# Performance work log

Measured on AMD Instinct MI355X. Metric: run time of the kernel, lower is better.

The kernel has to match this reference:

```python
import jax, jax.numpy as jnp
import numpy as np

DIM = 2048
DIM_HEAD = 64
HEADS = 16
FF_MULT = 4
LORA_R = 8
ATTN_INNER = DIM_HEAD * HEADS            # 1024
FF_INNER = DIM * FF_MULT                 # 8192
FUSED_DIMS = (ATTN_INNER, DIM_HEAD, DIM_HEAD, FF_INNER * 2)
B, N = 2, 2048


def setup_inputs() -> dict:
    key = jax.random.key(0)
    ks = jax.random.split(key, 12)
    s = 0.02
    inp = {
        "x": jax.random.normal(ks[0], (B, N, DIM), dtype=jnp.float32),
        "gamma": jnp.ones((DIM,), dtype=jnp.float32),
        "w_fused": jax.random.normal(ks[1], (DIM, sum(FUSED_DIMS)), dtype=jnp.float32) * s,
        "w_attn_out": jax.random.normal(ks[2], (ATTN_INNER, DIM), dtype=jnp.float32) * s,
        "w_ff_out": jax.random.normal(ks[3], (FF_INNER, DIM), dtype=jnp.float32) * s,
        "lora_q_a": jax.random.normal(ks[4], (DIM, LORA_R), dtype=jnp.float32) * s,
        "lora_q_b": jax.random.normal(ks[5], (LORA_R, ATTN_INNER), dtype=jnp.float32) * s,
        "lora_k_a": jax.random.normal(ks[6], (DIM, LORA_R), dtype=jnp.float32) * s,
        "lora_k_b": jax.random.normal(ks[7], (LORA_R, DIM_HEAD), dtype=jnp.float32) * s,
        "lora_v_a": jax.random.normal(ks[8], (DIM, LORA_R), dtype=jnp.float32) * s,
        "lora_v_b": jax.random.normal(ks[9], (LORA_R, DIM_HEAD), dtype=jnp.float32) * s,
        "lora_o_a": jax.random.normal(ks[10], (ATTN_INNER, LORA_R), dtype=jnp.float32) * s,
        "lora_o_b": jax.random.normal(ks[11], (LORA_R, DIM), dtype=jnp.float32) * s,
    }
    return inp


def _rotate_half(x):
    x1, x2 = jnp.split(x, 2, axis=-1)
    return jnp.concatenate((-x2, x1), axis=-1)


def _rope(pos, t):
    return t * jnp.cos(pos) + _rotate_half(t) * jnp.sin(pos)


def _forward(x, gamma, w_fused, w_attn_out, w_ff_out,
             lora_q_a, lora_q_b, lora_k_a, lora_k_b,
             lora_v_a, lora_v_b, lora_o_a, lora_o_b):
    b, n, d = x.shape
    # LayerNorm (beta = 0)
    mu = jnp.mean(x, axis=-1, keepdims=True)
    var = jnp.var(x, axis=-1, keepdims=True)
    xn = (x - mu) * jax.lax.rsqrt(var + 1e-5) * gamma

    fused = xn @ w_fused
    i0, i1, i2 = np.cumsum(FUSED_DIMS)[:3]
    q, k, v, ff = fused[..., :i0], fused[..., i0:i1], fused[..., i1:i2], fused[..., i2:]

    # LoRA additive terms
    q = q + (xn @ lora_q_a) @ lora_q_b
    k = k + (xn @ lora_k_a) @ lora_k_b
    v = v + (xn @ lora_v_a) @ lora_v_b

    q = q.reshape(b, n, HEADS, DIM_HEAD).transpose(0, 2, 1, 3)  # b h n d
    q = q * (DIM_HEAD ** -0.5)

    # rotary embedding: pos (n, dim_head)
    inv_freq = 1.0 / (10000.0 ** (jnp.arange(0, DIM_HEAD, 2, dtype=jnp.float32) / DIM_HEAD))
    freqs = jnp.arange(n, dtype=jnp.float32)[:, None] * inv_freq[None, :]
    pos = jnp.concatenate((freqs, freqs), axis=-1)
    q = _rope(pos, q)
    k = _rope(pos, k)  # k is b n d (multi-query, single kv head)

    sim = jnp.einsum('bhid,bjd->bhij', q, k)
    causal = jnp.triu(jnp.ones((n, n), dtype=bool), k=1)
    sim = jnp.where(causal, -jnp.finfo(sim.dtype).max, sim)
    attn = jax.nn.softmax(sim, axis=-1)
    out = jnp.einsum('bhij,bjd->bhid', attn, v)
    out = out.transpose(0, 2, 1, 3).reshape(b, n, ATTN_INNER)

    attn_out = out @ w_attn_out + (out @ lora_o_a) @ lora_o_b

    # SwiGLU: chunk -> (x_ff, gate); silu(gate) * x_ff
    x_ff, gate = jnp.split(ff, 2, axis=-1)
    ff_out = (jax.nn.silu(gate) * x_ff) @ w_ff_out

    return attn_out + ff_out


def reference(x, gamma, w_fused, w_attn_out, w_ff_out,
              lora_q_a, lora_q_b, lora_k_a, lora_k_b,
              lora_v_a, lora_v_b, lora_o_a, lora_o_b):
    return _forward(x, gamma, w_fused, w_attn_out, w_ff_out,
                    lora_q_a, lora_q_b, lora_k_a, lora_k_b,
                    lora_v_a, lora_v_b, lora_o_a, lora_o_b)
```

## Files before the change

### kernel.cpp

```cpp
#include <hip/hip_runtime.h>
#include <cstdint>


typedef __bf16 bf16_t;
typedef __bf16 bf16x8 __attribute__((ext_vector_type(8)));
typedef float f32x4 __attribute__((ext_vector_type(4)));

#define LOG2E 1.44269504088896340736f
#define LOG2_10K 13.287712379549449f

__device__ __forceinline__ void gload_lds16(const void* g, void* l) {
  __builtin_amdgcn_global_load_lds(
      (__attribute__((address_space(1))) void*)(uintptr_t)g,
      (__attribute__((address_space(3))) void*)(uint32_t)(uintptr_t)l,
      16, 0, 0);
}

__device__ __forceinline__ f32x4 mfma16(bf16x8 a, bf16x8 b, f32x4 c) {
  return __builtin_amdgcn_mfma_f32_16x16x32_bf16(a, b, c, 0, 0, 0);
}

__global__ __launch_bounds__(256) void ln_kernel(
    const float* __restrict__ x, const float* __restrict__ gamma,
    bf16_t* __restrict__ xn)
{
  const int row = blockIdx.x;
  const int t = threadIdx.x;
  const float4* xr = (const float4*)(x + (size_t)row * 2048);
  float4 a = xr[t * 2];
  float4 b = xr[t * 2 + 1];
  float s  = a.x + a.y + a.z + a.w + b.x + b.y + b.z + b.w;
  float ss = a.x*a.x + a.y*a.y + a.z*a.z + a.w*a.w
           + b.x*b.x + b.y*b.y + b.z*b.z + b.w*b.w;
  #pragma unroll
  for (int m = 1; m < 64; m <<= 1) {
    s  += __shfl_xor(s, m);
    ss += __shfl_xor(ss, m);
  }
  __shared__ float red[8];
  const int wave = t >> 6, lane = t & 63;
  if (lane == 0) { red[wave] = s; red[4 + wave] = ss; }
  __syncthreads();
  const float stot  = red[0] + red[1] + red[2] + red[3];
  const float sstot = red[4] + red[5] + red[6] + red[7];
  const float mu  = stot * (1.f / 2048.f);
  const float var = sstot * (1.f / 2048.f) - mu * mu;
  const float rs  = rsqrtf(var + 1e-5f);
  float v[8] = {a.x, a.y, a.z, a.w, b.x, b.y, b.z, b.w};
  bf16x8 o;
  #pragma unroll
  for (int e = 0; e < 8; ++e)
    o[e] = (bf16_t)((v[e] - mu) * rs * gamma[t * 8 + e]);
  *(bf16x8*)(xn + (size_t)row * 2048 + t * 8) = o;
}

__global__ __launch_bounds__(256) void transpose_wf_kernel(
    const float* __restrict__ w,
    const float* __restrict__ qa, const float* __restrict__ qb,
    const float* __restrict__ ka, const float* __restrict__ kb,
    const float* __restrict__ va, const float* __restrict__ vb,
    bf16_t* __restrict__ wfT)
{
  __shared__ float tile[64][65];
  const int t  = threadIdx.x;
  const int n0 = blockIdx.x * 64;
  const int k0 = blockIdx.y * 64;
  #pragma unroll
  for (int it = 0; it < 4; ++it) {
    const int kr = (t >> 4) + it * 16;
    const float4 vv = *(const float4*)(w + (size_t)(k0 + kr) * 17536 + n0 + (t & 15) * 4);
    tile[kr][(t & 15) * 4 + 0] = vv.x;
    tile[kr][(t & 15) * 4 + 1] = vv.y;
    tile[kr][(t & 15) * 4 + 2] = vv.z;
    tile[kr][(t & 15) * 4 + 3] = vv.w;
  }
  __syncthreads();
  const float* la = nullptr; const float* lb = nullptr;
  int nbo = 0, ldlb = 0;
  if (n0 < 1024)      { la = qa; lb = qb; nbo = n0;        ldlb = 1024; }
  else if (n0 < 1088) { la = ka; lb = kb; nbo = n0 - 1024; ldlb = 64;   }
  else if (n0 < 1152) { la = va; lb = vb; nbo = n0 - 1088; ldlb = 64;   }
  #pragma unroll
  for (int it = 0; it < 2; ++it) {
    const int nl = (t >> 3) + it * 32;
    const int kl = (t & 7) * 8;
    float vals[8];
    #pragma unroll
    for (int e = 0; e < 8; ++e) vals[e] = tile[kl + e][nl];
    if (la) {
      float bc[8];
      #pragma unroll
      for (int r = 0; r < 8; ++r) bc[r] = lb[r * ldlb + nbo + nl];
      #pragma unroll
      for (int e = 0; e < 8; ++e) {
        const float* ar = la + (size_t)(k0 + kl + e) * 8;
        float d = 0.f;
        #pragma unroll
        for (int r = 0; r < 8; ++r) d += ar[r] * bc[r];
        vals[e] += d;
      }
    }
    bf16x8 o;
    #pragma unroll
    for (int e = 0; e < 8; ++e) o[e] = (bf16_t)vals[e];
    *(bf16x8*)(wfT + (size_t)(n0 + nl) * 2048 + k0 + kl) = o;
  }
}

__global__ __launch_bounds__(256) void transpose_w2_kernel(
    const float* __restrict__ wff,
    const float* __restrict__ watt,
    const float* __restrict__ oa, const float* __restrict__ ob,
    bf16_t* __restrict__ w2T)
{
  __shared__ float tile[64][65];
  const int t  = threadIdx.x;
  const int n0 = blockIdx.x * 64;
  const int k0 = blockIdx.y * 64;
  const bool isatt = (k0 >= 8192);
  const float* src = isatt ? (watt + (size_t)(k0 - 8192) * 2048)
                           : (wff + (size_t)k0 * 2048);
  #pragma unroll
  for (int it = 0; it < 4; ++it) {
    const int kr = (t >> 4) + it * 16;
    const float4 vv = *(const float4*)(src + (size_t)kr * 2048 + n0 + (t & 15) * 4);
    tile[kr][(t & 15) * 4 + 0] = vv.x;
    tile[kr][(t & 15) * 4 + 1] = vv.y;
    tile[kr][(t & 15) * 4 + 2] = vv.z;
    tile[kr][(t & 15) * 4 + 3] = vv.w;
  }
  __syncthreads();
  #pragma unroll
  for (int it = 0; it < 2; ++it) {
    const int nl = (t >> 3) + it * 32;
    const int kl = (t & 7) * 8;
    float vals[8];
    #pragma unroll
    for (int e = 0; e < 8; ++e) vals[e] = tile[kl + e][nl];
    if (isatt) {
      float bc[8];
      #pragma unroll
      for (int r = 0; r < 8; ++r) bc[r] = ob[r * 2048 + n0 + nl];
      #pragma unroll
      for (int e = 0; e < 8; ++e) {
        const float* ar = oa + (size_t)(k0 - 8192 + kl + e) * 8;
        float d = 0.f;
        #pragma unroll
        for (int r = 0; r < 8; ++r) d += ar[r] * bc[r];
        vals[e] += d;
      }
    }
    bf16x8 o;
    #pragma unroll
    for (int e = 0; e < 8; ++e) o[e] = (bf16_t)vals[e];
    *(bf16x8*)(w2T + (size_t)(n0 + nl) * 9216 + k0 + kl) = o;
  }
}

__device__ __forceinline__ void gemm_core_128x128(
    const bf16_t* __restrict__ A, int ldA, int m0,
    const bf16_t* __restrict__ BT, int ldB, int n0,
    int K, bf16_t* As, bf16_t* Bs, f32x4* acc)
{
  const int t = threadIdx.x;
  const int wave = t >> 6;
  const int lane = t & 63;
  const int quad = lane >> 4;
  const int ln15 = lane & 15;
  const int wm = wave & 1, wn = wave >> 1;

  const bf16_t* gA = A + (size_t)(m0 + (t >> 2)) * ldA + ((t & 3) << 3);
  const bf16_t* gB = BT + (size_t)(n0 + (t >> 2)) * ldB + ((t & 3) << 3);
  char* lA = (char*)As + wave * 1024;
  char* lB = (char*)Bs + wave * 1024;
  const size_t sA64 = (size_t)64 * ldA;
  const size_t sB64 = (size_t)64 * ldB;
  const int aoff = (wm * 64 + ln15) * 32 + quad * 8;
  const int boff = (wn * 64 + ln15) * 32 + quad * 8;

  for (int kt = 0; kt < K; kt += 32) {
    gload_lds16(gA,        lA);
    gload_lds16(gA + sA64, lA + 4096);
    gload_lds16(gB,        lB);
    gload_lds16(gB + sB64, lB + 4096);
    gA += 32;
    gB += 32;
    __syncthreads();
    bf16x8 a0 = *(const bf16x8*)(As + aoff);
    bf16x8 a1 = *(const bf16x8*)(As + aoff + 512);
    bf16x8 a2 = *(const bf16x8*)(As + aoff + 1024);
    bf16x8 a3 = *(const bf16x8*)(As + aoff + 1536);
    bf16x8 b0 = *(const bf16x8*)(Bs + boff);
    bf16x8 b1 = *(const bf16x8*)(Bs + boff + 512);
    bf16x8 b2 = *(const bf16x8*)(Bs + boff + 1024);
    bf16x8 b3 = *(const bf16x8*)(Bs + boff + 1536);
    acc[0]  = mfma16(a0, b0, acc[0]);
    acc[1]  = mfma16(a0, b1, acc[1]);
    acc[2]  = mfma16(a0, b2, acc[2]);
    acc[3]  = mfma16(a0, b3, acc[3]);
    acc[4]  = mfma16(a1, b0, acc[4]);
    acc[5]  = mfma16(a1, b1, acc[5]);
    acc[6]  = mfma16(a1, b2, acc[6]);
    acc[7]  = mfma16(a1, b3, acc[7]);
    acc[8]  = mfma16(a2, b0, acc[8]);
    acc[9]  = mfma16(a2, b1, acc[9]);
    acc[10] = mfma16(a2, b2, acc[10]);
    acc[11] = mfma16(a2, b3, acc[11]);
    acc[12] = mfma16(a3, b0, acc[12]);
    acc[13] = mfma16(a3, b1, acc[13]);
    acc[14] = mfma16(a3, b2, acc[14]);
    acc[15] = mfma16(a3, b3, acc[15]);
    __syncthreads();
  }
}

__device__ __forceinline__ void gemm_core_dual(
    const bf16_t* gA, const bf16_t* gB0, const bf16_t* gB1,
    int ldA, int ldB, int K,
    bf16_t* As, bf16_t* B0s, bf16_t* B1s,
    f32x4* acc0, f32x4* acc1)
{
  const int t = threadIdx.x;
  const int wave = t >> 6;
  const int lane = t & 63;
  const int quad = lane >> 4;
  const int ln15 = lane & 15;
  const int wm = wave & 1, wn = wave >> 1;

  char* lA = (char*)As + wave * 1024;
  char* l0 = (char*)B0s + wave * 1024;
  char* l1 = (char*)B1s + wave * 1024;
  const size_t sA64 = (size_t)64 * ldA;
  const size_t sB64 = (size_t)64 * ldB;
  const int aoff = (wm * 64 + ln15) * 32 + quad * 8;
  const int boff = (wn * 64 + ln15) * 32 + quad * 8;

  for (int kt = 0; kt < K; kt += 32) {
    gload_lds16(gA,         lA);
    gload_lds16(gA + sA64,  lA + 4096);
    gload_lds16(gB0,        l0);
    gload_lds16(gB0 + sB64, l0 + 4096);
    gload_lds16(gB1,        l1);
    gload_lds16(gB1 + sB64, l1 + 4096);
    gA += 32; gB0 += 32; gB1 += 32;
    __syncthreads();
    bf16x8 a0 = *(const bf16x8*)(As + aoff);
    bf16x8 a1 = *(const bf16x8*)(As + aoff + 512);
    bf16x8 a2 = *(const bf16x8*)(As + aoff + 1024);
    bf16x8 a3 = *(const bf16x8*)(As + aoff + 1536);
    bf16x8 p0 = *(const bf16x8*)(B0s + boff);
    bf16x8 p1 = *(const bf16x8*)(B0s + boff + 512);
    bf16x8 p2 = *(const bf16x8*)(B0s + boff + 1024);
    bf16x8 p3 = *(const bf16x8*)(B0s + boff + 1536);
    bf16x8 q0 = *(const bf16x8*)(B1s + boff);
    bf16x8 q1 = *(const bf16x8*)(B1s + boff + 512);
    bf16x8 q2 = *(const bf16x8*)(B1s + boff + 1024);
    bf16x8 q3 = *(const bf16x8*)(B1s + boff + 1536);
    acc0[0]  = mfma16(a0, p0, acc0[0]);
    acc0[1]  = mfma16(a0, p1, acc0[1]);
    acc0[2]  = mfma16(a0, p2, acc0[2]);
    acc0[3]  = mfma16(a0, p3, acc0[3]);
    acc1[0]  = mfma16(a0, q0, acc1[0]);
    acc1[1]  = mfma16(a0, q1, acc1[1]);
    acc1[2]  = mfma16(a0, q2, acc1[2]);
    acc1[3]  = mfma16(a0, q3, acc1[3]);
    acc0[4]  = mfma16(a1, p0, acc0[4]);
    acc0[5]  = mfma16(a1, p1, acc0[5]);
    acc0[6]  = mfma16(a1, p2, acc0[6]);
    acc0[7]  = mfma16(a1, p3, acc0[7]);
    acc1[4]  = mfma16(a1, q0, acc1[4]);
    acc1[5]  = mfma16(a1, q1, acc1[5]);
    acc1[6]  = mfma16(a1, q2, acc1[6]);
    acc1[7]  = mfma16(a1, q3, acc1[7]);
    acc0[8]  = mfma16(a2, p0, acc0[8]);
    acc0[9]  = mfma16(a2, p1, acc0[9]);
    acc0[10] = mfma16(a2, p2, acc0[10]);
    acc0[11] = mfma16(a2, p3, acc0[11]);
    acc1[8]  = mfma16(a2, q0, acc1[8]);
    acc1[9]  = mfma16(a2, q1, acc1[9]);
    acc1[10] = mfma16(a2, q2, acc1[10]);
    acc1[11] = mfma16(a2, q3, acc1[11]);
    acc0[12] = mfma16(a3, p0, acc0[12]);
    acc0[13] = mfma16(a3, p1, acc0[13]);
    acc0[14] = mfma16(a3, p2, acc0[14]);
    acc0[15] = mfma16(a3, p3, acc0[15]);
    acc1[12] = mfma16(a3, q0, acc1[12]);
    acc1[13] = mfma16(a3, q1, acc1[13]);
    acc1[14] = mfma16(a3, q2, acc1[14]);
    acc1[15] = mfma16(a3, q3, acc1[15]);
    __syncthreads();
  }
}

__global__ __launch_bounds__(256, 2) void gemm1_qkv_kernel(
    const bf16_t* __restrict__ xn, const bf16_t* __restrict__ wfT,
    bf16_t* __restrict__ Q, bf16_t* __restrict__ K, bf16_t* __restrict__ Vt)
{
  __shared__ __align__(16) bf16_t As[128 * 32];
  __shared__ __align__(16) bf16_t B0s[128 * 32];
  __shared__ __align__(16) bf16_t B1s[128 * 32];
  const int m0 = blockIdx.x * 128;
  const int y = blockIdx.y;
  const int t = threadIdx.x;
  const int wave = t >> 6, lane = t & 63;
  const int quad = lane >> 4, ln15 = lane & 15;
  const int wm = wave & 1, wn = wave >> 1;

  const int rb = m0 + wm * 64 + quad * 4;
  const float invf0 = exp2f(-(float)ln15 * (LOG2_10K / 32.0f));
  const float invf1 = exp2f(-(float)(16 + ln15) * (LOG2_10K / 32.0f));

  if (y < 4) {
    const bf16_t* gA  = xn  + (size_t)(m0 + (t >> 2)) * 2048 + ((t & 3) << 3);
    const bf16_t* gB0 = wfT + (size_t)(y * 256 + (t >> 2)) * 2048 + ((t & 3) << 3);
    const bf16_t* gB1 = wfT + (size_t)(y * 256 + 128 + (t >> 2)) * 2048 + ((t & 3) << 3);
    f32x4 acc0[16], acc1[16];
    #pragma unroll
    for (int f = 0; f < 16; ++f) {
      acc0[f] = (f32x4){0.f, 0.f, 0.f, 0.f};
      acc1[f] = (f32x4){0.f, 0.f, 0.f, 0.f};
    }
    gemm_core_dual(gA, gB0, gB1, 2048, 2048, 2048, As, B0s, B1s, acc0, acc1);
    #pragma unroll
    for (int half = 0; half < 2; ++half) {
      const f32x4* acc = half ? acc1 : acc0;
      const int hd = y * 4 + half * 2 + wn;
      #pragma unroll
      for (int i = 0; i < 4; ++i) {
        #pragma unroll
        for (int rr = 0; rr < 4; ++rr) {
          const int row = rb + i * 16 + rr;
          const int b = row >> 11, n = row & 2047;
          const float fn = (float)n;
          float s0, c0, s1, c1;
          __sincosf(fn * invf0, &s0, &c0);
          __sincosf(fn * invf1, &s1, &c1);
          float vals[4];
          #pragma unroll
          for (int j = 0; j < 4; ++j) vals[j] = acc[i * 4 + j][rr];
          #pragma unroll
          for (int j = 0; j < 4; ++j) {
            const float rot = (j < 2) ? -vals[j + 2] : vals[j - 2];
            const float c = (j & 1) ? c1 : c0;
            const float s = (j & 1) ? s1 : s0;
            const float o = (vals[j] * c + rot * s) * 0.125f;
            Q[(((size_t)b * 16 + hd) * 2048 + n) * 64 + j * 16 + ln15] = (bf16_t)o;
          }
        }
      }
    }
  } else {
    f32x4 acc[16];
    #pragma unroll
    for (int f = 0; f < 16; ++f) acc[f] = (f32x4){0.f, 0.f, 0.f, 0.f};
    gemm_core_128x128(xn, 2048, m0, wfT, 2048, 1024, 2048, As, B0s, acc);
    const bool is_k = (wn == 0);
    #pragma unroll
    for (int i = 0; i < 4; ++i) {
      #pragma unroll
      for (int rr = 0; rr < 4; ++rr) {
        const int row = rb + i * 16 + rr;
        const int b = row >> 11, n = row & 2047;
        float vals[4];
        #pragma unroll
        for (int j = 0; j < 4; ++j) vals[j] = acc[i * 4 + j][rr];
        if (is_k) {
          const float fn = (float)n;
          float s0, c0, s1, c1;
          __sincosf(fn * invf0, &s0, &c0);
          __sincosf(fn * invf1, &s1, &c1);
          #pragma unroll
          for (int j = 0; j < 4; ++j) {
            const float rot = (j < 2) ? -vals[j + 2] : vals[j - 2];
            const float c = (j & 1) ? c1 : c0;
            const float s = (j & 1) ? s1 : s0;
            K[((size_t)b * 2048 + n) * 64 + j * 16 + ln15] = (bf16_t)(vals[j] * c + rot * s);
          }
        } else {
          #pragma unroll
          for (int j = 0; j < 4; ++j)
            Vt[((size_t)b * 64 + j * 16 + ln15) * 2048 + n] = (bf16_t)vals[j];
        }
      }
    }
  }
}

__global__ __launch_bounds__(256, 2) void gemm1_ff_kernel(
    const bf16_t* __restrict__ xn, const bf16_t* __restrict__ wfT,
    bf16_t* __restrict__ A2, int m_base)
{
  __shared__ __align__(16) bf16_t As[128 * 32];
  __shared__ __align__(16) bf16_t Bg[128 * 32];
  __shared__ __align__(16) bf16_t Bx[128 * 32];
  const int m0 = m_base + blockIdx.x * 128;
  const int c  = blockIdx.y;
  const int t = threadIdx.x;
  const int wave = t >> 6, lane = t & 63;
  const int quad = lane >> 4, ln15 = lane & 15;
  const int wm = wave & 1, wn = wave >> 1;

  const bf16_t* gA = xn  + (size_t)(m0 + (t >> 2)) * 2048 + ((t & 3) << 3);
  const bf16_t* gG = wfT + (size_t)(9344 + c * 128 + (t >> 2)) * 2048 + ((t & 3) << 3);
  const bf16_t* gX = wfT + (size_t)(1152 + c * 128 + (t >> 2)) * 2048 + ((t & 3) << 3);

  f32x4 accg[16], accx[16];
  #pragma unroll
  for (int f = 0; f < 16; ++f) {
    accg[f] = (f32x4){0.f, 0.f, 0.f, 0.f};
    accx[f] = (f32x4){0.f, 0.f, 0.f, 0.f};
  }
  gemm_core_dual(gA, gG, gX, 2048, 2048, 2048, As, Bg, Bx, accg, accx);

  const int rb = m0 + wm * 64 + quad * 4;
  const int cb = c * 128 + wn * 64 + ln15;
  #pragma unroll
  for (int i = 0; i < 4; ++i)
    #pragma unroll
    for (int rr = 0; rr < 4; ++rr) {
      bf16_t* dst = A2 + (size_t)(rb + i * 16 + rr) * 9216 + cb;
      #pragma unroll
      for (int j = 0; j < 4; ++j) {
        const float g = accg[i * 4 + j][rr];
        const float xv = accx[i * 4 + j][rr];
        dst[j * 16] = (bf16_t)(xv * (g / (1.f + exp2f(-g * LOG2E))));
      }
    }
}

__global__ __launch_bounds__(256, 2) void gemm2_kernel(
    const bf16_t* __restrict__ A2, const bf16_t* __restrict__ w2T,
    float* __restrict__ out)
{
  __shared__ __align__(16) bf16_t As[128 * 32];
  __shared__ __align__(16) bf16_t B0[128 * 32];
  __shared__ __align__(16) bf16_t B1[128 * 32];
  const int m0 = blockIdx.x * 128;
  const int n0 = blockIdx.y * 256;
  const int k0 = blockIdx.z * 4608;
  const int t = threadIdx.x;
  const int wave = t >> 6, lane = t & 63;
  const int quad = lane >> 4, ln15 = lane & 15;
  const int wm = wave & 1, wn = wave >> 1;

  const bf16_t* gA  = A2  + (size_t)(m0 + (t >> 2)) * 9216 + k0 + ((t & 3) << 3);
  const bf16_t* gB0 = w2T + (size_t)(n0 + (t >> 2)) * 9216 + k0 + ((t & 3) << 3);
  const bf16_t* gB1 = w2T + (size_t)(n0 + 128 + (t >> 2)) * 9216 + k0 + ((t & 3) << 3);

  f32x4 acc0[16], acc1[16];
  #pragma unroll
  for (int f = 0; f < 16; ++f) {
    acc0[f] = (f32x4){0.f, 0.f, 0.f, 0.f};
    acc1[f] = (f32x4){0.f, 0.f, 0.f, 0.f};
  }
  gemm_core_dual(gA, gB0, gB1, 9216, 9216, 4608, As, B0, B1, acc0, acc1);

  const int rb = m0 + wm * 64 + quad * 4;
  #pragma unroll
  for (int half = 0; half < 2; ++half) {
    const f32x4* acc = half ? acc1 : acc0;
    const int cb = n0 + half * 128 + wn * 64 + ln15;
    #pragma unroll
    for (int i = 0; i < 4; ++i)
      #pragma unroll
      for (int rr = 0; rr < 4; ++rr) {
        float* dst = out + (size_t)(rb + i * 16 + rr) * 2048 + cb;
        #pragma unroll
        for (int j = 0; j < 4; ++j)
          unsafeAtomicAdd(dst + j * 16, acc[i * 4 + j][rr]);
      }
  }
}

__global__ __launch_bounds__(256, 2) void attn_kernel(
    const bf16_t* __restrict__ Q, const bf16_t* __restrict__ Kg_,
    const bf16_t* __restrict__ Vt, bf16_t* __restrict__ A2)
{
  __shared__ __align__(16) bf16_t Qs[64 * 64];
  __shared__ __align__(16) bf16_t Ks[64 * 64];
  __shared__ __align__(16) bf16_t Vs[64 * 64];
  __shared__ __align__(16) bf16_t Ps[64 * 64];
  const int pidx = blockIdx.x, bh = blockIdx.y;
  const int b = bh >> 4, h = bh & 15;
  const int t = threadIdx.x;
  const int wave = t >> 6, lane = t & 63;
  const int quad = lane >> 4, ln15 = lane & 15;

  const bf16_t* Kg = Kg_ + (size_t)b * 2048 * 64;
  const bf16_t* Vg = Vt + (size_t)b * 64 * 2048;

  for (int hlf = 0; hlf < 2; ++hlf) {
    const int qt = hlf ? (31 - pidx) : pidx;
    const int qm0 = qt * 64;
    const bf16_t* Qg = Q + ((size_t)bh * 2048 + qm0) * 64;

    {
      const bf16_t* g = Qg + (size_t)(t >> 3) * 64 + ((t & 7) << 3);
      char* l = (char*)Qs + wave * 1024;
      gload_lds16(g,           l);
      gload_lds16(g + 32 * 64, l + 4096);
    }

    float mstate[4], lstate[4];
    f32x4 o_acc[4];
    #pragma unroll
    for (int rr = 0; rr < 4; ++rr) { mstate[rr] = -1e30f; lstate[rr] = 0.f; }
    #pragma unroll
    for (int jd = 0; jd < 4; ++jd) o_acc[jd] = (f32x4){0.f, 0.f, 0.f, 0.f};

    const int njt = qt + 1;
    for (int jt = 0; jt < njt; ++jt) {
      {
        const bf16_t* kg = Kg + (size_t)(jt * 64 + (t >> 3)) * 64 + ((t & 7) << 3);
        char* lk = (char*)Ks + wave * 1024;
        gload_lds16(kg,           lk);
        gload_lds16(kg + 32 * 64, lk + 4096);
        const bf16_t* vg = Vg + (size_t)(t >> 3) * 2048 + jt * 64 + ((t & 7) << 3);
        char* lv = (char*)Vs + wave * 1024;
        gload_lds16(vg,                   lv);
        gload_lds16(vg + (size_t)32*2048, lv + 4096);
      }
      __syncthreads();

      f32x4 sA[4];
      #pragma unroll
      for (int j = 0; j < 4; ++j) sA[j] = (f32x4){0.f, 0.f, 0.f, 0.f};
      #pragma unroll
      for (int ks = 0; ks < 2; ++ks) {
        bf16x8 aq = *(const bf16x8*)(Qs + (wave * 16 + ln15) * 64 + ks * 32 + quad * 8);
        #pragma unroll
        for (int j = 0; j < 4; ++j) {
          bf16x8 bk = *(const bf16x8*)(Ks + (j * 16 + ln15) * 64 + ks * 32 + quad * 8);
          sA[j] = mfma16(aq, bk, sA[j]);
        }
      }

      const bool needmask = (jt * 64 + 63 > qm0 + wave * 16);
      const int row0 = qm0 + wave * 16 + quad * 4;
      float alpha[4];
      #pragma unroll
      for (int rr = 0; rr < 4; ++rr) {
        const int rowg = row0 + rr;
        if (needmask) {
          #pragma unroll
          for (int j = 0; j < 4; ++j) {
            const int colg = jt * 64 + j * 16 + ln15;
            if (colg > rowg) sA[j][rr] = -1e30f;
          }
        }
        float mx = fmaxf(fmaxf(sA[0][rr], sA[1][rr]),
                         fmaxf(sA[2][rr], sA[3][rr]));
        mx = fmaxf(mx, __shfl_xor(mx, 1));
        mx = fmaxf(mx, __shfl_xor(mx, 2));
        mx = fmaxf(mx, __shfl_xor(mx, 4));
        mx = fmaxf(mx, __shfl_xor(mx, 8));
        const float mold = mstate[rr];
        const float mnew = fmaxf(mold, mx);
        const float al = exp2f((mold - mnew) * LOG2E);
        float rsum = 0.f;
        #pragma unroll
        for (int j = 0; j < 4; ++j) {
          const float p = exp2f((sA[j][rr] - mnew) * LOG2E);
          sA[j][rr] = p;
          rsum += p;
        }
        rsum += __shfl_xor(rsum, 1);
        rsum += __shfl_xor(rsum, 2);
        rsum += __shfl_xor(rsum, 4);
        rsum += __shfl_xor(rsum, 8);
        lstate[rr] = lstate[rr] * al + rsum;
        mstate[rr] = mnew;
        alpha[rr] = al;
      }
      #pragma unroll
      for (int jd = 0; jd < 4; ++jd)
        #pragma unroll
        for (int rr = 0; rr < 4; ++rr)
          o_acc[jd][rr] *= alpha[rr];
      #pragma unroll
      for (int j = 0; j < 4; ++j)
        #pragma unroll
        for (int rr = 0; rr < 4; ++rr)
          Ps[wave * 1024 + (quad * 4 + rr) * 64 + j * 16 + ln15] = (bf16_t)sA[j][rr];

      #pragma unroll
      for (int ks = 0; ks < 2; ++ks) {
        bf16x8 ap = *(const bf16x8*)(Ps + wave * 1024 + ln15 * 64 + ks * 32 + quad * 8);
        #pragma unroll
        for (int jd = 0; jd < 4; ++jd) {
          bf16x8 bv = *(const bf16x8*)(Vs + (jd * 16 + ln15) * 64 + ks * 32 + quad * 8);
          o_acc[jd] = mfma16(ap, bv, o_acc[jd]);
        }
      }
      __syncthreads();
    }

    const int row0 = qm0 + wave * 16 + quad * 4;
    #pragma unroll
    for (int rr = 0; rr < 4; ++rr) {
      const float inv = 1.f / lstate[rr];
      bf16_t* dst = A2 + ((size_t)b * 2048 + row0 + rr) * 9216 + 8192 + h * 64 + ln15;
      #pragma unroll
      for (int jd = 0; jd < 4; ++jd)
        dst[jd * 16] = (bf16_t)(o_acc[jd][rr] * inv);
    }
  }
}

extern "C" void kernel_launch(void* const* d_in, const int* in_sizes, int n_in,
                              void* d_out, int out_size, void* d_ws, size_t ws_size,
                              hipStream_t stream)
{
  const float* x      = (const float*)d_in[0];
  const float* gamma  = (const float*)d_in[1];
  const float* wfused = (const float*)d_in[2];
  const float* watt   = (const float*)d_in[3];
  const float* wff    = (const float*)d_in[4];
  const float* qa     = (const float*)d_in[5];
  const float* qb     = (const float*)d_in[6];
  const float* ka     = (const float*)d_in[7];
  const float* kb     = (const float*)d_in[8];
  const float* va     = (const float*)d_in[9];
  const float* vb     = (const float*)d_in[10];
  const float* oa     = (const float*)d_in[11];
  const float* ob     = (const float*)d_in[12];
  float* out = (float*)d_out;

  char* ws = (char*)d_ws;
  bf16_t* xn  = (bf16_t*)(ws);
  bf16_t* wfT = (bf16_t*)(ws + 16777216);
  bf16_t* w2T = (bf16_t*)(ws + 88604672);
  bf16_t* A2  = (bf16_t*)(ws + 126353408);
  bf16_t* Qr  = (bf16_t*)(ws + 201850880);
  bf16_t* Kr  = (bf16_t*)(ws + 210239488);
  bf16_t* Vtr = (bf16_t*)(ws + 210763776);

  hipMemsetAsync(d_out, 0, (size_t)out_size * sizeof(float), stream);

  ln_kernel<<<dim3(4096), dim3(256), 0, stream>>>(x, gamma, xn);
  transpose_wf_kernel<<<dim3(274, 32), dim3(256), 0, stream>>>(
      wfused, qa, qb, ka, kb, va, vb, wfT);
  transpose_w2_kernel<<<dim3(32, 144), dim3(256), 0, stream>>>(
      wff, watt, oa, ob, w2T);
  gemm1_qkv_kernel<<<dim3(32, 5), dim3(256), 0, stream>>>(xn, wfT, Qr, Kr, Vtr);
  gemm1_ff_kernel<<<dim3(16, 64), dim3(256), 0, stream>>>(xn, wfT, A2, 0);
  gemm1_ff_kernel<<<dim3(16, 64), dim3(256), 0, stream>>>(xn, wfT, A2, 2048);
  attn_kernel<<<dim3(16, 32), dim3(256), 0, stream>>>(Qr, Kr, Vtr, A2);
  gemm2_kernel<<<dim3(32, 8, 2), dim3(256), 0, stream>>>(A2, w2T, out);
}
```

Before: 964.4 us.

## Rewrite FF and output GEMMs with 256-row tiles, 4-stage LDS pipeline, no split-K

Both large GEMMs now use 512-thread blocks with 256-row M tiles and a 4-stage global-to-LDS pipeline driven by direct global_load_lds. The pipeline uses XOR-swizzled LDS layouts, raised wave priority around the MFMA blocks, and interleaved gate/x columns so each wave holds matching SwiGLU pairs. The two FF launches merge into one. The output GEMM drops split-K and its atomics in favour of plain stores, which also removes the memset of the output. The cost is large LDS use (128KB and 96KB per block), which limits occupancy, and fewer blocks in the output GEMM (256).

```diff
diff --git a/kernel.cpp b/kernel.cpp
--- a/kernel.cpp
+++ b/kernel.cpp
@@ -386,90 +386,192 @@
   }
 }
 
-__global__ __launch_bounds__(256, 2) void gemm1_ff_kernel(
+__global__ __launch_bounds__(512, 2) void gemm1_ff_kernel(
     const bf16_t* __restrict__ xn, const bf16_t* __restrict__ wfT,
-    bf16_t* __restrict__ A2, int m_base)
-{
-  __shared__ __align__(16) bf16_t As[128 * 32];
-  __shared__ __align__(16) bf16_t Bg[128 * 32];
-  __shared__ __align__(16) bf16_t Bx[128 * 32];
-  const int m0 = m_base + blockIdx.x * 128;
-  const int c  = blockIdx.y;
+    bf16_t* __restrict__ A2)
+{
+  __shared__ __align__(16) char lds[131072];
+  const int m0 = blockIdx.x * 256;
+  const int c0 = blockIdx.y * 128;
   const int t = threadIdx.x;
-  const int wave = t >> 6, lane = t & 63;
+  const int w = t >> 6, lane = t & 63;
   const int quad = lane >> 4, ln15 = lane & 15;
-  const int wm = wave & 1, wn = wave >> 1;
-
-  const bf16_t* gA = xn  + (size_t)(m0 + (t >> 2)) * 2048 + ((t & 3) << 3);
-  const bf16_t* gG = wfT + (size_t)(9344 + c * 128 + (t >> 2)) * 2048 + ((t & 3) << 3);
-  const bf16_t* gX = wfT + (size_t)(1152 + c * 128 + (t >> 2)) * 2048 + ((t & 3) << 3);
-
-  f32x4 accg[16], accx[16];
-  #pragma unroll
-  for (int f = 0; f < 16; ++f) {
-    accg[f] = (f32x4){0.f, 0.f, 0.f, 0.f};
-    accx[f] = (f32x4){0.f, 0.f, 0.f, 0.f};
-  }
-  gemm_core_dual(gA, gG, gX, 2048, 2048, 2048, As, Bg, Bx, accg, accx);
-
-  const int rb = m0 + wm * 64 + quad * 4;
-  const int cb = c * 128 + wn * 64 + ln15;
-  #pragma unroll
-  for (int i = 0; i < 4; ++i)
+  const int wm = w & 1, wn = w >> 1;
+
+  const int p  = w * 64 + lane;
+  const int r  = p >> 2;
+  const int cl = (p & 3) ^ ((r >> 1) & 3);
+  const bf16_t* gA = xn + (size_t)(m0 + r) * 2048 + cl * 8;
+  const int r2 = r + 128;
+  const int cm0 = c0 + ((r  >> 5) << 4) + (r  & 15);
+  const int cm1 = c0 + ((r2 >> 5) << 4) + (r2 & 15);
+  const int wr0 = ((r  >> 4) & 1) ? (1152 + cm0) : (9344 + cm0);
+  const int wr1 = ((r2 >> 4) & 1) ? (1152 + cm1) : (9344 + cm1);
+  const bf16_t* gB0 = wfT + (size_t)wr0 * 2048 + cl * 8;
+  const bf16_t* gB1 = wfT + (size_t)wr1 * 2048 + cl * 8;
+
+  const int ro = ln15 * 64 + ((quad ^ ((ln15 >> 1) & 3)) * 16);
+
+  f32x4 acc[8][4];
+  #pragma unroll
+  for (int mf = 0; mf < 8; ++mf)
+    #pragma unroll
+    for (int nf = 0; nf < 4; ++nf)
+      acc[mf][nf] = (f32x4){0.f, 0.f, 0.f, 0.f};
+
+  #pragma unroll
+  for (int pt = 0; pt < 3; ++pt) {
+    char* lA = lds + pt * 16384 + w * 1024;
+    gload_lds16(gA,                        lA);
+    gload_lds16(gA + (size_t)128 * 2048,   lA + 8192);
+    char* lB = lds + 65536 + pt * 16384 + w * 1024;
+    gload_lds16(gB0, lB);
+    gload_lds16(gB1, lB + 8192);
+    gA += 32; gB0 += 32; gB1 += 32;
+  }
+  asm volatile("s_waitcnt vmcnt(8)" ::: "memory");
+  __builtin_amdgcn_s_barrier();
+
+  for (int tt = 0; tt < 64; ++tt) {
+    const int s  = tt & 3;
+    const int s3 = (tt + 3) & 3;
+    const bool st = (tt < 61);
+    bf16x8 a[4], b[4];
+    #pragma unroll
+    for (int mf = 0; mf < 4; ++mf)
+      a[mf] = *(const bf16x8*)(lds + s * 16384 + wm * 8192 + mf * 1024 + ro);
+    #pragma unroll
+    for (int nf = 0; nf < 4; ++nf)
+      b[nf] = *(const bf16x8*)(lds + 65536 + s * 16384 + wn * 4096 + nf * 1024 + ro);
+    if (st) {
+      char* lA = lds + s3 * 16384 + w * 1024;
+      gload_lds16(gA,                      lA);
+      gload_lds16(gA + (size_t)128 * 2048, lA + 8192);
+    }
+    __builtin_amdgcn_s_barrier();
+    __builtin_amdgcn_s_setprio(1);
+    #pragma unroll
+    for (int mf = 0; mf < 4; ++mf)
+      #pragma unroll
+      for (int nf = 0; nf < 4; ++nf)
+        acc[mf][nf] = mfma16(a[mf], b[nf], acc[mf][nf]);
+    __builtin_amdgcn_s_setprio(0);
+    bf16x8 a2[4];
+    #pragma unroll
+    for (int mf = 0; mf < 4; ++mf)
+      a2[mf] = *(const bf16x8*)(lds + s * 16384 + wm * 8192 + (4 + mf) * 1024 + ro);
+    if (st) {
+      char* lB = lds + 65536 + s3 * 16384 + w * 1024;
+      gload_lds16(gB0, lB);
+      gload_lds16(gB1, lB + 8192);
+      gA += 32; gB0 += 32; gB1 += 32;
+    }
+    __builtin_amdgcn_s_barrier();
+    __builtin_amdgcn_s_setprio(1);
+    #pragma unroll
+    for (int mf = 0; mf < 4; ++mf)
+      #pragma unroll
+      for (int nf = 0; nf < 4; ++nf)
+        acc[4 + mf][nf] = mfma16(a2[mf], b[nf], acc[4 + mf][nf]);
+    __builtin_amdgcn_s_setprio(0);
+    asm volatile("s_waitcnt vmcnt(8)" ::: "memory");
+    __builtin_amdgcn_s_barrier();
+  }
+
+  const int row0 = m0 + wm * 128 + quad * 4;
+  const int col0 = c0 + wn * 32 + ln15;
+  #pragma unroll
+  for (int mf = 0; mf < 8; ++mf)
     #pragma unroll
     for (int rr = 0; rr < 4; ++rr) {
-      bf16_t* dst = A2 + (size_t)(rb + i * 16 + rr) * 9216 + cb;
-      #pragma unroll
-      for (int j = 0; j < 4; ++j) {
-        const float g = accg[i * 4 + j][rr];
-        const float xv = accx[i * 4 + j][rr];
+      bf16_t* dst = A2 + (size_t)(row0 + mf * 16 + rr) * 9216 + col0;
+      #pragma unroll
+      for (int j = 0; j < 2; ++j) {
+        const float g  = acc[mf][2 * j][rr];
+        const float xv = acc[mf][2 * j + 1][rr];
         dst[j * 16] = (bf16_t)(xv * (g / (1.f + exp2f(-g * LOG2E))));
       }
     }
 }
 
-__global__ __launch_bounds__(256, 2) void gemm2_kernel(
+__global__ __launch_bounds__(512, 2) void gemm2_kernel(
     const bf16_t* __restrict__ A2, const bf16_t* __restrict__ w2T,
     float* __restrict__ out)
 {
-  __shared__ __align__(16) bf16_t As[128 * 32];
-  __shared__ __align__(16) bf16_t B0[128 * 32];
-  __shared__ __align__(16) bf16_t B1[128 * 32];
-  const int m0 = blockIdx.x * 128;
-  const int n0 = blockIdx.y * 256;
-  const int k0 = blockIdx.z * 4608;
+  __shared__ __align__(16) char lds[98304];
+  const int m0 = blockIdx.x * 256;
+  const int n0 = blockIdx.y * 128;
   const int t = threadIdx.x;
-  const int wave = t >> 6, lane = t & 63;
+  const int w = t >> 6, lane = t & 63;
   const int quad = lane >> 4, ln15 = lane & 15;
-  const int wm = wave & 1, wn = wave >> 1;
-
-  const bf16_t* gA  = A2  + (size_t)(m0 + (t >> 2)) * 9216 + k0 + ((t & 3) << 3);
-  const bf16_t* gB0 = w2T + (size_t)(n0 + (t >> 2)) * 9216 + k0 + ((t & 3) << 3);
-  const bf16_t* gB1 = w2T + (size_t)(n0 + 128 + (t >> 2)) * 9216 + k0 + ((t & 3) << 3);
-
-  f32x4 acc0[16], acc1[16];
-  #pragma unroll
-  for (int f = 0; f < 16; ++f) {
-    acc0[f] = (f32x4){0.f, 0.f, 0.f, 0.f};
-    acc1[f] = (f32x4){0.f, 0.f, 0.f, 0.f};
-  }
-  gemm_core_dual(gA, gB0, gB1, 9216, 9216, 4608, As, B0, B1, acc0, acc1);
-
-  const int rb = m0 + wm * 64 + quad * 4;
-  #pragma unroll
-  for (int half = 0; half < 2; ++half) {
-    const f32x4* acc = half ? acc1 : acc0;
-    const int cb = n0 + half * 128 + wn * 64 + ln15;
-    #pragma unroll
-    for (int i = 0; i < 4; ++i)
-      #pragma unroll
-      for (int rr = 0; rr < 4; ++rr) {
-        float* dst = out + (size_t)(rb + i * 16 + rr) * 2048 + cb;
-        #pragma unroll
-        for (int j = 0; j < 4; ++j)
-          unsafeAtomicAdd(dst + j * 16, acc[i * 4 + j][rr]);
-      }
-  }
+  const int wm = w & 3, wn = w >> 2;
+
+  const int p  = w * 64 + lane;
+  const int r  = p >> 2;
+  const int cl = (p & 3) ^ ((r >> 1) & 3);
+  const bf16_t* gA = A2  + (size_t)(m0 + r) * 9216 + cl * 8;
+  const bf16_t* gB = w2T + (size_t)(n0 + r) * 9216 + cl * 8;
+
+  const int ro = ln15 * 64 + ((quad ^ ((ln15 >> 1) & 3)) * 16);
+
+  f32x4 acc[4][4];
+  #pragma unroll
+  for (int mf = 0; mf < 4; ++mf)
+    #pragma unroll
+    for (int nf = 0; nf < 4; ++nf)
+      acc[mf][nf] = (f32x4){0.f, 0.f, 0.f, 0.f};
+
+  #pragma unroll
+  for (int pt = 0; pt < 3; ++pt) {
+    char* lA = lds + pt * 16384 + w * 1024;
+    gload_lds16(gA,                      lA);
+    gload_lds16(gA + (size_t)128 * 9216, lA + 8192);
+    gload_lds16(gB, lds + 65536 + pt * 8192 + w * 1024);
+    gA += 32; gB += 32;
+  }
+  asm volatile("s_waitcnt vmcnt(6)" ::: "memory");
+  __builtin_amdgcn_s_barrier();
+
+  for (int tt = 0; tt < 288; ++tt) {
+    const int s = tt & 3;
+    bf16x8 a[4], b[4];
+    #pragma unroll
+    for (int mf = 0; mf < 4; ++mf)
+      a[mf] = *(const bf16x8*)(lds + s * 16384 + wm * 4096 + mf * 1024 + ro);
+    #pragma unroll
+    for (int nf = 0; nf < 4; ++nf)
+      b[nf] = *(const bf16x8*)(lds + 65536 + s * 8192 + wn * 4096 + nf * 1024 + ro);
+    if (tt < 285) {
+      const int s3 = (tt + 3) & 3;
+      char* lA = lds + s3 * 16384 + w * 1024;
+      gload_lds16(gA,                      lA);
+      gload_lds16(gA + (size_t)128 * 9216, lA + 8192);
+      gload_lds16(gB, lds + 65536 + s3 * 8192 + w * 1024);
+      gA += 32; gB += 32;
+    }
+    __builtin_amdgcn_s_barrier();
+    __builtin_amdgcn_s_setprio(1);
+    #pragma unroll
+    for (int mf = 0; mf < 4; ++mf)
+      #pragma unroll
+      for (int nf = 0; nf < 4; ++nf)
+        acc[mf][nf] = mfma16(a[mf], b[nf], acc[mf][nf]);
+    __builtin_amdgcn_s_setprio(0);
+    asm volatile("s_waitcnt vmcnt(6)" ::: "memory");
+    __builtin_amdgcn_s_barrier();
+  }
+
+  const int row0 = m0 + wm * 64 + quad * 4;
+  const int col0 = n0 + wn * 64 + ln15;
+  #pragma unroll
+  for (int mf = 0; mf < 4; ++mf)
+    #pragma unroll
+    for (int rr = 0; rr < 4; ++rr) {
+      float* dst = out + (size_t)(row0 + mf * 16 + rr) * 2048 + col0;
+      #pragma unroll
+      for (int nf = 0; nf < 4; ++nf)
+        dst[nf * 16] = acc[mf][nf][rr];
+    }
 }
 
 __global__ __launch_bounds__(256, 2) void attn_kernel(
@@ -635,16 +737,13 @@
   bf16_t* Kr  = (bf16_t*)(ws + 210239488);
   bf16_t* Vtr = (bf16_t*)(ws + 210763776);
 
-  hipMemsetAsync(d_out, 0, (size_t)out_size * sizeof(float), stream);
-
   ln_kernel<<<dim3(4096), dim3(256), 0, stream>>>(x, gamma, xn);
   transpose_wf_kernel<<<dim3(274, 32), dim3(256), 0, stream>>>(
       wfused, qa, qb, ka, kb, va, vb, wfT);
   transpose_w2_kernel<<<dim3(32, 144), dim3(256), 0, stream>>>(
       wff, watt, oa, ob, w2T);
   gemm1_qkv_kernel<<<dim3(32, 5), dim3(256), 0, stream>>>(xn, wfT, Qr, Kr, Vtr);
-  gemm1_ff_kernel<<<dim3(16, 64), dim3(256), 0, stream>>>(xn, wfT, A2, 0);
-  gemm1_ff_kernel<<<dim3(16, 64), dim3(256), 0, stream>>>(xn, wfT, A2, 2048);
+  gemm1_ff_kernel<<<dim3(16, 64), dim3(512), 0, stream>>>(xn, wfT, A2);
   attn_kernel<<<dim3(16, 32), dim3(256), 0, stream>>>(Qr, Kr, Vtr, A2);
-  gemm2_kernel<<<dim3(32, 8, 2), dim3(256), 0, stream>>>(A2, w2T, out);
-}
+  gemm2_kernel<<<dim3(16, 16), dim3(512), 0, stream>>>(A2, w2T, out);
+}
```

New measurement: 876.8 us. 1.1x faster.
